# Optimization experiments

Measured on AMD Instinct MI355X. Metric: run time of the kernel, lower is better.

The kernel has to match this reference:

```python
import jax, jax.numpy as jnp
import numpy as np

L, Q = 256, 21
LAMBDA_H = 1e-06
LAMBDA_J = 0.0001
M = 8192


def setup_inputs() -> dict:
    key = jax.random.key(0)
    k1, k2, k3, k4 = jax.random.split(key, 4)
    seqs = jax.random.randint(k1, (M, L), 0, Q, dtype=jnp.int64 if jax.config.jax_enable_x64 else jnp.int32)
    weights = jax.random.uniform(k2, (M,), dtype=jnp.float32)
    h = jax.random.normal(k3, (L, Q), dtype=jnp.float32) * 0.1
    J = jax.random.normal(k4, (L, L, Q, Q), dtype=jnp.float32) * 0.02
    return {"seqs": seqs, "weights": weights, "h": h, "J": J}


def reference(seqs, weights, h, J):
    # strictly-lower-triangular mask over (i, j): j < i
    tril = jnp.tril(jnp.ones((L, L), dtype=bool), k=-1)
    Jm = J * tril[:, :, None, None]                       # (L, L, q, q)

    # one-hot history; H[b, j, k] = 1 iff seqs[b, j] == k
    H = jax.nn.one_hot(seqs, Q, dtype=h.dtype)            # (M, L, q)

    # contrib[b, i, a] = sum_{j<i, k} J[i, j, a, k] * H[b, j, k]
    # == one big (M, L*q) x (L*q, L*q) causal-masked matmul
    contrib = jnp.einsum('ijak,bjk->bia', Jm, H)          # (M, L, q)

    logits = h[None, :, :] + contrib                      # (M, L, q)
    logp = jax.nn.log_softmax(logits, axis=-1)            # (M, L, q)

    # gather label log-probs
    ll = jnp.take_along_axis(logp, seqs[..., None], axis=-1)[..., 0]  # (M, L)

    M_eff = jnp.maximum(weights.sum(), 1e-12)
    w_norm = weights / M_eff
    nll = -(w_norm[:, None] * ll).sum()

    reg_h = 0.5 * LAMBDA_H * jnp.sum(h ** 2)
    reg_J = 0.5 * LAMBDA_J * jnp.sum(Jm ** 2)
    loss = nll + reg_h + reg_J
    return (loss, nll, reg_h + reg_J)
```

## Files before the change

kernel.cpp:

```cpp
#include <hip/hip_runtime.h>
#include <cstdint>
#include <cstddef>

#define L_   256
#define Q_   21
#define M_   8192
#define QQ   441
#define JCH  32
#define SCALE    32.0f
#define INVSCALE 0.03125f
#define NPAIR ((L_ * (L_ - 1)) / 2)
#define PREPB 2048


typedef float v2f __attribute__((ext_vector_type(2)));

__device__ __forceinline__ float block_reduce_sum(float v) {
    __shared__ float s[256];
    int t = threadIdx.x;
    s[t] = v;
    __syncthreads();
#pragma unroll
    for (int o = 128; o > 0; o >>= 1) {
        if (t < o) s[t] += s[t + o];
        __syncthreads();
    }
    return s[0];
}

__global__ void k_wsum_h2(const float* __restrict__ w, const float* __restrict__ h,
                          float* __restrict__ acc) {
    int t = threadIdx.x;
    float v = 0.f;
    for (int x = t; x < M_; x += 256) v += w[x];
    float r = block_reduce_sum(v);
    if (t == 0) acc[0] = r;
    float v2 = 0.f;
    for (int x = t; x < L_ * Q_; x += 256) { float y = h[x]; v2 += y * y; }
    float r2 = block_reduce_sum(v2);
    if (t == 0) acc[2] = r2;
}

__global__ void k_pack_seqs(const int* __restrict__ seqs, unsigned* __restrict__ seqsP) {
    int b = blockIdx.x * 256 + threadIdx.x;
    const int4* row = reinterpret_cast<const int4*>(seqs + (size_t)b * L_);
#pragma unroll 4
    for (int jq = 0; jq < L_ / 4; ++jq) {
        int4 v = row[jq];
        unsigned p = (unsigned)(v.x & 255) | ((unsigned)(v.y & 255) << 8) |
                     ((unsigned)(v.z & 255) << 16) | ((unsigned)(v.w & 255) << 24);
        seqsP[jq * M_ + b] = p;
    }
}

__global__ __launch_bounds__(256) void k_prep_J(const float* __restrict__ J,
                                                unsigned* __restrict__ Jt,
                                                float* __restrict__ acc) {
    __shared__ float sB[QQ];
    int t = threadIdx.x;
    float v2acc = 0.f;

    for (int n = blockIdx.x; n < NPAIR; n += PREPB) {
        int i = (int)((1.0f + sqrtf(8.0f * (float)n + 1.0f)) * 0.5f);
        while (i * (i - 1) / 2 > n) --i;
        while (i * (i - 1) / 2 + i <= n) ++i;
        int j = n - i * (i - 1) / 2;
        const size_t ij = (size_t)i * L_ + j;

        const float* blk = J + ij * QQ;
        for (int x = t; x < QQ; x += 256) sB[x] = blk[x];
        __syncthreads();

        if (t < 128) {
            int k  = t / 6;
            int dw = t - 6 * k;
            int a0 = dw * 4;
            unsigned outw = 0;
            if (k < Q_) {
                float x0 = (a0 + 0 < Q_) ? sB[(a0 + 0) * Q_ + k] : 0.f;
                float x1 = (a0 + 1 < Q_) ? sB[(a0 + 1) * Q_ + k] : 0.f;
                float x2 = (a0 + 2 < Q_) ? sB[(a0 + 2) * Q_ + k] : 0.f;
                float x3 = (a0 + 3 < Q_) ? sB[(a0 + 3) * Q_ + k] : 0.f;
                v2acc += x0 * x0 + x1 * x1 + x2 * x2 + x3 * x3;
                outw = (unsigned)__builtin_amdgcn_cvt_pk_fp8_f32(x0 * SCALE, x1 * SCALE, 0, false);
                outw = (unsigned)__builtin_amdgcn_cvt_pk_fp8_f32(x2 * SCALE, x3 * SCALE, (int)outw, true);
            }
            Jt[ij * 128 + t] = outw;
        }
        __syncthreads();
    }

    float r = block_reduce_sum(v2acc);
    if (t == 0) atomicAdd(&acc[4 + (blockIdx.x & 63)], r);
}

__global__ __launch_bounds__(256, 4) void k_main(const unsigned* __restrict__ Jt,
                                                 const float* __restrict__ h,
                                                 const unsigned* __restrict__ seqsP,
                                                 const float* __restrict__ weights,
                                                 float* __restrict__ acc) {
    __shared__ unsigned sJ[JCH * 128];

    const int bid = blockIdx.x;
    const int i = (L_ - 1) - (bid >> 5);
    const int b = ((bid & 31) << 8) + threadIdx.x;

    v2f acc2[11];
    const float* hp = h + i * Q_;
#pragma unroll
    for (int m = 0; m < 10; ++m) { acc2[m].x = hp[2*m] * SCALE; acc2[m].y = hp[2*m+1] * SCALE; }
    acc2[10].x = hp[20] * SCALE; acc2[10].y = 0.f;

    const unsigned* Jrow = Jt + (size_t)i * (256 * 128);

    for (int j0 = 0; j0 < i; j0 += JCH) {
        {
            const uint4* src = reinterpret_cast<const uint4*>(Jrow + j0 * 128);
            uint4* dst = reinterpret_cast<uint4*>(sJ);
#pragma unroll
            for (int n = 0; n < (JCH * 32) / 256; ++n) {
                dst[n * 256 + threadIdx.x] = src[n * 256 + threadIdx.x];
            }
        }
        __syncthreads();

        unsigned idxw[JCH / 4];
#pragma unroll
        for (int q = 0; q < JCH / 4; ++q) {
            idxw[q] = seqsP[((j0 >> 2) + q) * M_ + b];
        }

        const int nj = min(i - j0, JCH);
#pragma unroll
        for (int jj = 0; jj < JCH; ++jj) {
            if (jj >= nj) break;
            const unsigned k = (idxw[jj >> 2] >> ((jj & 3) * 8)) & 255u;
            const uint2* r = reinterpret_cast<const uint2*>(sJ) + (jj * 64 + k * 3);
            uint2 d0 = r[0], d1 = r[1], d2 = r[2];
            acc2[0]  += __builtin_amdgcn_cvt_pk_f32_fp8(d0.x, false);
            acc2[1]  += __builtin_amdgcn_cvt_pk_f32_fp8(d0.x, true);
            acc2[2]  += __builtin_amdgcn_cvt_pk_f32_fp8(d0.y, false);
            acc2[3]  += __builtin_amdgcn_cvt_pk_f32_fp8(d0.y, true);
            acc2[4]  += __builtin_amdgcn_cvt_pk_f32_fp8(d1.x, false);
            acc2[5]  += __builtin_amdgcn_cvt_pk_f32_fp8(d1.x, true);
            acc2[6]  += __builtin_amdgcn_cvt_pk_f32_fp8(d1.y, false);
            acc2[7]  += __builtin_amdgcn_cvt_pk_f32_fp8(d1.y, true);
            acc2[8]  += __builtin_amdgcn_cvt_pk_f32_fp8(d2.x, false);
            acc2[9]  += __builtin_amdgcn_cvt_pk_f32_fp8(d2.x, true);
            acc2[10] += __builtin_amdgcn_cvt_pk_f32_fp8(d2.y, false);
        }
        __syncthreads();
    }

    float l[21];
#pragma unroll
    for (int m = 0; m < 10; ++m) { l[2*m] = acc2[m].x * INVSCALE; l[2*m+1] = acc2[m].y * INVSCALE; }
    l[20] = acc2[10].x * INVSCALE;

    unsigned lw = seqsP[(i >> 2) * M_ + b];
    int lbl = (int)((lw >> ((i & 3) * 8)) & 255u);

    float m = l[0];
#pragma unroll
    for (int a = 1; a < 21; ++a) m = fmaxf(m, l[a]);
    float s = 0.f;
    float lv = l[0];
#pragma unroll
    for (int a = 0; a < 21; ++a) {
        s += __expf(l[a] - m);
        if (a > 0) lv = (a == lbl) ? l[a] : lv;
    }
    float ll = (lv - m) - __logf(s);
    float contrib = weights[b] * ll;

    float r = block_reduce_sum(contrib);
    if (threadIdx.x == 0) atomicAdd(&acc[1], r);
}

__global__ void k_final(const float* __restrict__ acc, float* __restrict__ out) {
    if (threadIdx.x == 0 && blockIdx.x == 0) {
        float wsum = fmaxf(acc[0], 1e-12f);
        float nll = -acc[1] / wsum;
        float j2 = 0.f;
        for (int s = 0; s < 64; ++s) j2 += acc[4 + s];
        float reg = 0.5e-6f * acc[2] + 0.5e-4f * j2;
        out[0] = nll + reg;
        out[1] = nll;
        out[2] = reg;
    }
}

extern "C" void kernel_launch(void* const* d_in, const int* in_sizes, int n_in,
                              void* d_out, int out_size, void* d_ws, size_t ws_size,
                              hipStream_t stream) {
    const int*   seqs    = (const int*)d_in[0];
    const float* weights = (const float*)d_in[1];
    const float* h       = (const float*)d_in[2];
    const float* J       = (const float*)d_in[3];
    float* out = (float*)d_out;

    char* ws = (char*)d_ws;
    float*    acc   = (float*)ws;
    unsigned* seqsP = (unsigned*)(ws + 512);
    unsigned* Jt    = (unsigned*)(ws + 512 + (size_t)(L_ / 4) * M_ * sizeof(unsigned));

    hipMemsetAsync(d_ws, 0, 512, stream);

    k_wsum_h2<<<1, 256, 0, stream>>>(weights, h, acc);
    k_pack_seqs<<<M_ / 256, 256, 0, stream>>>(seqs, seqsP);
    k_prep_J<<<PREPB, 256, 0, stream>>>(J, Jt, acc);

    k_main<<<L_ * (M_ / 256), 256, 0, stream>>>(Jt, h, seqsP, weights, acc);

    k_final<<<1, 1, 0, stream>>>(acc, out);
}
```

Measured before the change: 453.3 us.

## Fuse prep kernels into one launch, spread atomics, raise main occupancy hint

Merges the weight-sum, sequence-packing and J-conversion kernels into a single launch, with block ranges dispatched to each role, and gives each J block exactly four pairs. The main kernel's launch bound moves to 8 waves per SIMD, and its per-block NLL atomics are spread over 128 slots instead of one contended address, which the final kernel reduces in parallel. The aim is to cut launch overhead and atomic contention and to improve latency hiding. The tighter register budget could cause spills in the main loop.

```diff
diff --git a/kernel.cpp b/kernel.cpp
--- a/kernel.cpp
+++ b/kernel.cpp
@@ -10,7 +10,7 @@
 #define SCALE    32.0f
 #define INVSCALE 0.03125f
 #define NPAIR ((L_ * (L_ - 1)) / 2)
-#define PREPB 2048
+#define PREPB 8160
 
 
 typedef float v2f __attribute__((ext_vector_type(2)));
@@ -18,6 +18,7 @@
 __device__ __forceinline__ float block_reduce_sum(float v) {
     __shared__ float s[256];
     int t = threadIdx.x;
+    __syncthreads();
     s[t] = v;
     __syncthreads();
 #pragma unroll
@@ -28,73 +29,75 @@
     return s[0];
 }
 
-__global__ void k_wsum_h2(const float* __restrict__ w, const float* __restrict__ h,
-                          float* __restrict__ acc) {
-    int t = threadIdx.x;
-    float v = 0.f;
-    for (int x = t; x < M_; x += 256) v += w[x];
-    float r = block_reduce_sum(v);
-    if (t == 0) acc[0] = r;
-    float v2 = 0.f;
-    for (int x = t; x < L_ * Q_; x += 256) { float y = h[x]; v2 += y * y; }
-    float r2 = block_reduce_sum(v2);
-    if (t == 0) acc[2] = r2;
-}
-
-__global__ void k_pack_seqs(const int* __restrict__ seqs, unsigned* __restrict__ seqsP) {
-    int b = blockIdx.x * 256 + threadIdx.x;
-    const int4* row = reinterpret_cast<const int4*>(seqs + (size_t)b * L_);
+__global__ __launch_bounds__(256) void k_prep(const float* __restrict__ J,
+                                              const int* __restrict__ seqs,
+                                              const float* __restrict__ w,
+                                              const float* __restrict__ h,
+                                              unsigned* __restrict__ Jt,
+                                              unsigned* __restrict__ seqsP,
+                                              float* __restrict__ acc) {
+    const int bid = blockIdx.x;
+    const int t = threadIdx.x;
+
+    if (bid < PREPB) {
+        __shared__ float sB[QQ];
+        float v2acc = 0.f;
+#pragma unroll 1
+        for (int q = 0; q < 4; ++q) {
+            const int n = bid * 4 + q;
+            int i = (int)((1.0f + sqrtf(8.0f * (float)n + 1.0f)) * 0.5f);
+            while (i * (i - 1) / 2 > n) --i;
+            while (i * (i - 1) / 2 + i <= n) ++i;
+            const int j = n - i * (i - 1) / 2;
+            const size_t ij = (size_t)i * L_ + j;
+
+            const float* blk = J + ij * QQ;
+            for (int x = t; x < QQ; x += 256) sB[x] = blk[x];
+            __syncthreads();
+
+            if (t < 128) {
+                int k  = t / 6;
+                int dw = t - 6 * k;
+                int a0 = dw * 4;
+                unsigned outw = 0;
+                if (k < Q_) {
+                    float x0 = (a0 + 0 < Q_) ? sB[(a0 + 0) * Q_ + k] : 0.f;
+                    float x1 = (a0 + 1 < Q_) ? sB[(a0 + 1) * Q_ + k] : 0.f;
+                    float x2 = (a0 + 2 < Q_) ? sB[(a0 + 2) * Q_ + k] : 0.f;
+                    float x3 = (a0 + 3 < Q_) ? sB[(a0 + 3) * Q_ + k] : 0.f;
+                    v2acc += x0 * x0 + x1 * x1 + x2 * x2 + x3 * x3;
+                    outw = (unsigned)__builtin_amdgcn_cvt_pk_fp8_f32(x0 * SCALE, x1 * SCALE, 0, false);
+                    outw = (unsigned)__builtin_amdgcn_cvt_pk_fp8_f32(x2 * SCALE, x3 * SCALE, (int)outw, true);
+                }
+                Jt[ij * 128 + t] = outw;
+            }
+            __syncthreads();
+        }
+        float r = block_reduce_sum(v2acc);
+        if (t == 0) atomicAdd(&acc[4 + (bid & 255)], r);
+    } else if (bid < PREPB + 32) {
+        const int b = (bid - PREPB) * 256 + t;
+        const int4* row = reinterpret_cast<const int4*>(seqs + (size_t)b * L_);
 #pragma unroll 4
-    for (int jq = 0; jq < L_ / 4; ++jq) {
-        int4 v = row[jq];
-        unsigned p = (unsigned)(v.x & 255) | ((unsigned)(v.y & 255) << 8) |
-                     ((unsigned)(v.z & 255) << 16) | ((unsigned)(v.w & 255) << 24);
-        seqsP[jq * M_ + b] = p;
-    }
-}
-
-__global__ __launch_bounds__(256) void k_prep_J(const float* __restrict__ J,
-                                                unsigned* __restrict__ Jt,
-                                                float* __restrict__ acc) {
-    __shared__ float sB[QQ];
-    int t = threadIdx.x;
-    float v2acc = 0.f;
-
-    for (int n = blockIdx.x; n < NPAIR; n += PREPB) {
-        int i = (int)((1.0f + sqrtf(8.0f * (float)n + 1.0f)) * 0.5f);
-        while (i * (i - 1) / 2 > n) --i;
-        while (i * (i - 1) / 2 + i <= n) ++i;
-        int j = n - i * (i - 1) / 2;
-        const size_t ij = (size_t)i * L_ + j;
-
-        const float* blk = J + ij * QQ;
-        for (int x = t; x < QQ; x += 256) sB[x] = blk[x];
-        __syncthreads();
-
-        if (t < 128) {
-            int k  = t / 6;
-            int dw = t - 6 * k;
-            int a0 = dw * 4;
-            unsigned outw = 0;
-            if (k < Q_) {
-                float x0 = (a0 + 0 < Q_) ? sB[(a0 + 0) * Q_ + k] : 0.f;
-                float x1 = (a0 + 1 < Q_) ? sB[(a0 + 1) * Q_ + k] : 0.f;
-                float x2 = (a0 + 2 < Q_) ? sB[(a0 + 2) * Q_ + k] : 0.f;
-                float x3 = (a0 + 3 < Q_) ? sB[(a0 + 3) * Q_ + k] : 0.f;
-                v2acc += x0 * x0 + x1 * x1 + x2 * x2 + x3 * x3;
-                outw = (unsigned)__builtin_amdgcn_cvt_pk_fp8_f32(x0 * SCALE, x1 * SCALE, 0, false);
-                outw = (unsigned)__builtin_amdgcn_cvt_pk_fp8_f32(x2 * SCALE, x3 * SCALE, (int)outw, true);
-            }
-            Jt[ij * 128 + t] = outw;
-        }
-        __syncthreads();
-    }
-
-    float r = block_reduce_sum(v2acc);
-    if (t == 0) atomicAdd(&acc[4 + (blockIdx.x & 63)], r);
-}
-
-__global__ __launch_bounds__(256, 4) void k_main(const unsigned* __restrict__ Jt,
+        for (int jq = 0; jq < L_ / 4; ++jq) {
+            int4 v = row[jq];
+            unsigned p = (unsigned)(v.x & 255) | ((unsigned)(v.y & 255) << 8) |
+                         ((unsigned)(v.z & 255) << 16) | ((unsigned)(v.w & 255) << 24);
+            seqsP[jq * M_ + b] = p;
+        }
+    } else {
+        float v = 0.f;
+        for (int x = t; x < M_; x += 256) v += w[x];
+        float r = block_reduce_sum(v);
+        if (t == 0) acc[0] = r;
+        float v2 = 0.f;
+        for (int x = t; x < L_ * Q_; x += 256) { float y = h[x]; v2 += y * y; }
+        float r2 = block_reduce_sum(v2);
+        if (t == 0) acc[2] = r2;
+    }
+}
+
+__global__ __launch_bounds__(256, 8) void k_main(const unsigned* __restrict__ Jt,
                                                  const float* __restrict__ h,
                                                  const unsigned* __restrict__ seqsP,
                                                  const float* __restrict__ weights,
@@ -174,15 +177,18 @@
     float contrib = weights[b] * ll;
 
     float r = block_reduce_sum(contrib);
-    if (threadIdx.x == 0) atomicAdd(&acc[1], r);
+    if (threadIdx.x == 0) atomicAdd(&acc[260 + (bid & 127)], r);
 }
 
 __global__ void k_final(const float* __restrict__ acc, float* __restrict__ out) {
-    if (threadIdx.x == 0 && blockIdx.x == 0) {
+    int t = threadIdx.x;
+    float j2p = acc[4 + t];
+    float j2 = block_reduce_sum(j2p);
+    float llp = (t < 128) ? acc[260 + t] : 0.f;
+    float lls = block_reduce_sum(llp);
+    if (t == 0) {
         float wsum = fmaxf(acc[0], 1e-12f);
-        float nll = -acc[1] / wsum;
-        float j2 = 0.f;
-        for (int s = 0; s < 64; ++s) j2 += acc[4 + s];
+        float nll = -lls / wsum;
         float reg = 0.5e-6f * acc[2] + 0.5e-4f * j2;
         out[0] = nll + reg;
         out[1] = nll;
@@ -201,16 +207,12 @@
 
     char* ws = (char*)d_ws;
     float*    acc   = (float*)ws;
-    unsigned* seqsP = (unsigned*)(ws + 512);
-    unsigned* Jt    = (unsigned*)(ws + 512 + (size_t)(L_ / 4) * M_ * sizeof(unsigned));
-
-    hipMemsetAsync(d_ws, 0, 512, stream);
-
-    k_wsum_h2<<<1, 256, 0, stream>>>(weights, h, acc);
-    k_pack_seqs<<<M_ / 256, 256, 0, stream>>>(seqs, seqsP);
-    k_prep_J<<<PREPB, 256, 0, stream>>>(J, Jt, acc);
-
+    unsigned* seqsP = (unsigned*)(ws + 2048);
+    unsigned* Jt    = (unsigned*)(ws + 2048 + (size_t)(L_ / 4) * M_ * sizeof(unsigned));
+
+    hipMemsetAsync(d_ws, 0, 2048, stream);
+
+    k_prep<<<PREPB + 33, 256, 0, stream>>>(J, seqs, weights, h, Jt, seqsP, acc);
     k_main<<<L_ * (M_ / 256), 256, 0, stream>>>(Jt, h, seqsP, weights, acc);
-
-    k_final<<<1, 1, 0, stream>>>(acc, out);
-}
+    k_final<<<1, 256, 0, stream>>>(acc, out);
+}
```

Result: faster. 423.9 us (-6.5%).
